# Performance work log

Measured on AMD Instinct MI355X. Metric: run time of the kernel, lower is better.

## Reference

```python
import jax, jax.numpy as jnp
import numpy as np

N = 131072          # total sampled proposals (flattened over batch)
D = 1024            # num_extractor_out
C = 21              # num_classes (VOC: 20 + background)


def setup_inputs() -> dict:
    key = jax.random.key(0)
    k1, k2, k3 = jax.random.split(key, 3)
    features = jax.random.normal(k1, (N, D), dtype=jnp.float32)
    # Linear weights stored as [in, out] so y = x @ W + b
    W_cls = jax.random.normal(k2, (D, C), dtype=jnp.float32) * (1.0 / np.sqrt(D))
    b_cls = jnp.zeros((C,), dtype=jnp.float32)
    W_tf = jax.random.normal(k3, (D, C * 4), dtype=jnp.float32) * (1.0 / np.sqrt(D))
    b_tf = jnp.zeros((C * 4,), dtype=jnp.float32)
    return {"features": features, "W_cls": W_cls, "b_cls": b_cls, "W_tf": W_tf, "b_tf": b_tf}


def reference(features, W_cls, b_cls, W_tf, b_tf):
    # ROI.forward with identity extractor / no pre/post transforms.
    proposal_classes = features @ W_cls + b_cls                    # [N, C]
    proposal_transformers = features @ W_tf + b_tf                 # [N, C*4]
    proposal_transformers = proposal_transformers.reshape(features.shape[0], C, 4)
    return proposal_classes, proposal_transformers
```

## Files before the change

### kernel.cpp

```cpp
#include <hip/hip_runtime.h>
#include <hip/hip_bf16.h>

#define NROWS 131072
#define DK    1024
#define CCLS  21
#define CTF   84
#define NCOL  105
#define NCT   7
#define BM    16
#define SLABF 256
#define NSLAB (DK / SLABF)

typedef __attribute__((ext_vector_type(4))) float f32x4;
typedef __attribute__((ext_vector_type(8))) short bf16x8;
typedef __attribute__((ext_vector_type(2))) unsigned int u32x2;

__device__ __forceinline__ unsigned short f2bf_rne(float x) {
    union { float f; unsigned u; } v; v.f = x;
    unsigned r = v.u + 0x7fffu + ((v.u >> 16) & 1u);
    return (unsigned short)(r >> 16);
}

__device__ __forceinline__ unsigned pack2(float lo, float hi) {
    union { float f; unsigned u; } a, b; a.f = lo; b.f = hi;
    return ((a.u + 0x8000u) >> 16) | ((b.u + 0x8000u) & 0xffff0000u);
}

__global__ void pack_B_kernel(const float* __restrict__ Wc,
                              const float* __restrict__ Wt,
                              unsigned short* __restrict__ Bp) {
    const int frag = blockIdx.x;
    const int kt = frag / NCT, ct = frag % NCT;
    const int lane = threadIdx.x;
    const int col = ct * 16 + (lane & 15);
    const int k0  = kt * 32 + ((lane >> 4) << 3);
    bf16x8 o;
#pragma unroll
    for (int j = 0; j < 8; ++j) {
        const int k = k0 + j;
        float v = 0.0f;
        if (col < CCLS)      v = Wc[k * CCLS + col];
        else if (col < NCOL) v = Wt[k * CTF + (col - CCLS)];
        o[j] = (short)f2bf_rne(v);
    }
    *reinterpret_cast<bf16x8*>(Bp + ((size_t)frag * 64 + lane) * 8) = o;
}

__global__ __launch_bounds__(256, 4)
void roi_gemm_kernel(const float* __restrict__ F,
                     const unsigned short* __restrict__ Bp,
                     const float* __restrict__ bcls,
                     const float* __restrict__ btf,
                     float* __restrict__ out) {
    __shared__ __align__(16) unsigned char smem[28672];

    const int t    = threadIdx.x;
    const int wave = t >> 6;
    const int lane = t & 63;
    const int fr   = lane & 15;
    const int fq   = lane >> 4;
    const long rw  = (long)blockIdx.x * BM;

    const unsigned short* bb = Bp + (size_t)lane * 8;
    const float* abase = F + (size_t)(rw + wave * 4) * DK + lane * 4;

    f32x4 acc[NCT];
#pragma unroll
    for (int ct = 0; ct < NCT; ++ct) acc[ct] = (f32x4){0.f, 0.f, 0.f, 0.f};

#define AWADDR(BUF, Q) (smem + (BUF) * 8192 + (wave * 4 + (Q)) * 512 +        \
    (((lane >> 1) ^ ((wave * 4 + (Q)) & 7)) << 4) + ((lane & 1) << 3))

    {
        f32x4 v0[4];
#pragma unroll
        for (int q = 0; q < 4; ++q)
            v0[q] = *reinterpret_cast<const f32x4*>(abase + (size_t)q * DK);
#pragma unroll
        for (int q = 0; q < 4; ++q) {
            u32x2 d;
            d[0] = pack2(v0[q][0], v0[q][1]);
            d[1] = pack2(v0[q][2], v0[q][3]);
            *reinterpret_cast<u32x2*>(AWADDR(0, q)) = d;
        }
    }
    __syncthreads();

#pragma unroll
    for (int s = 0; s < NSLAB; ++s) {
        const int buf = s & 1;

        bf16x8 bfr[2][NCT];
#pragma unroll
        for (int jj = 0; jj < 2; ++jj) {
            const int ktg = s * 8 + wave * 2 + jj;
#pragma unroll
            for (int ct = 0; ct < NCT; ++ct)
                bfr[jj][ct] = *reinterpret_cast<const bf16x8*>(
                    bb + ((size_t)(ktg * NCT + ct) * 512));
        }
        __builtin_amdgcn_sched_barrier(0);

        f32x4 v[4];
        if (s + 1 < NSLAB) {
#pragma unroll
            for (int q = 0; q < 4; ++q)
                v[q] = *reinterpret_cast<const f32x4*>(
                    abase + (size_t)q * DK + (s + 1) * SLABF);
        }
        __builtin_amdgcn_sched_barrier(0);

#pragma unroll
        for (int jj = 0; jj < 2; ++jj) {
            const int lt = wave * 2 + jj;
            const bf16x8 a = *reinterpret_cast<const bf16x8*>(
                smem + buf * 8192 + fr * 512 +
                ((((lt << 2) | fq) ^ (fr & 7)) << 4));
#pragma unroll
            for (int ct = 0; ct < NCT; ++ct)
                acc[ct] = __builtin_amdgcn_mfma_f32_16x16x32_bf16(
                    a, bfr[jj][ct], acc[ct], 0, 0, 0);
        }
        __builtin_amdgcn_sched_barrier(0);

        if (s + 1 < NSLAB) {
#pragma unroll
            for (int q = 0; q < 4; ++q) {
                u32x2 d;
                d[0] = pack2(v[q][0], v[q][1]);
                d[1] = pack2(v[q][2], v[q][3]);
                *reinterpret_cast<u32x2*>(AWADDR(buf ^ 1, q)) = d;
            }
        }
        __syncthreads();
    }
#undef AWADDR

    float* sf = reinterpret_cast<float*>(smem);
#pragma unroll
    for (int ct = 0; ct < NCT; ++ct)
        *reinterpret_cast<f32x4*>(sf + ((wave * NCT + ct) << 8) + (lane << 2)) =
            acc[ct];
    __syncthreads();

    const int rcol0 = (t >> 2) & 15;
    float* out_tf = out + (size_t)NROWS * CCLS;
    const long grow = rw + ((t >> 6) << 2) + (t & 3);
#pragma unroll
    for (int ct = 0; ct < NCT; ++ct) {
        const int col = ct * 16 + rcol0;
        if (col >= NCOL) continue;
        const float v = sf[(0 * NCT + ct) * 256 + t] +
                        sf[(1 * NCT + ct) * 256 + t] +
                        sf[(2 * NCT + ct) * 256 + t] +
                        sf[(3 * NCT + ct) * 256 + t] +
                        ((col < CCLS) ? bcls[col] : btf[col - CCLS]);
        if (col < CCLS) out[grow * CCLS + col] = v;
        else            out_tf[grow * CTF + (col - CCLS)] = v;
    }
}

extern "C" void kernel_launch(void* const* d_in, const int* in_sizes, int n_in,
                              void* d_out, int out_size, void* d_ws, size_t ws_size,
                              hipStream_t stream) {
    const float* F  = (const float*)d_in[0];
    const float* Wc = (const float*)d_in[1];
    const float* bc = (const float*)d_in[2];
    const float* Wt = (const float*)d_in[3];
    const float* bt = (const float*)d_in[4];
    unsigned short* Bp = (unsigned short*)d_ws;

    pack_B_kernel<<<NCT * (DK / 32), 64, 0, stream>>>(Wc, Wt, Bp);
    roi_gemm_kernel<<<NROWS / BM, 256, 0, stream>>>(F, Bp, bc, bt,
                                                    (float*)d_out);
}
```

Before: 145.1 us.

## Deepen software pipeline with smaller K slabs and prefetched B fragments

Halves the K slab to 128 so each wave handles one k-tile per slab, and restructures the main loop into an explicitly unrolled two-stage pipeline. A loads are issued two slabs ahead and B fragments one slab ahead in ping-pong registers, while the bf16 conversion writes to LDS happen after the MFMAs. The full __syncthreads is replaced by an lgkmcnt wait plus s_barrier. The goal is to hide global memory latency of this bandwidth-bound skinny GEMM behind the MFMAs, at the cost of more barriers per K and higher register pressure.

```diff
diff --git a/kernel.cpp b/kernel.cpp
--- a/kernel.cpp
+++ b/kernel.cpp
@@ -8,7 +8,7 @@
 #define NCOL  105
 #define NCT   7
 #define BM    16
-#define SLABF 256
+#define SLABF 128
 #define NSLAB (DK / SLABF)
 
 typedef __attribute__((ext_vector_type(4))) float f32x4;
@@ -62,80 +62,98 @@
     const long rw  = (long)blockIdx.x * BM;
 
     const unsigned short* bb = Bp + (size_t)lane * 8;
-    const float* abase = F + (size_t)(rw + wave * 4) * DK + lane * 4;
+    const float* asrc = F + (size_t)(rw + wave * 4 + (lane >> 5)) * DK
+                        + (lane & 31) * 4;
+
+    const int c   = (lane & 31) >> 1;
+    const int h8  = (lane & 1) << 3;
+    const int R0  = wave * 4 + (lane >> 5);
+    const int R1  = R0 + 2;
+    const int w0  = R0 * 256 + (((c) ^ (R0 & 7)) << 4) + h8;
+    const int w1  = R1 * 256 + (((c) ^ (R1 & 7)) << 4) + h8;
+    const int rdoff = fr * 256 + (((wave * 4 + fq) ^ (fr & 7)) << 4);
 
     f32x4 acc[NCT];
 #pragma unroll
     for (int ct = 0; ct < NCT; ++ct) acc[ct] = (f32x4){0.f, 0.f, 0.f, 0.f};
 
-#define AWADDR(BUF, Q) (smem + (BUF) * 8192 + (wave * 4 + (Q)) * 512 +        \
-    (((lane >> 1) ^ ((wave * 4 + (Q)) & 7)) << 4) + ((lane & 1) << 3))
+    f32x4 vP[2], vQ[2];
+    bf16x8 bfrP[NCT], bfrQ[NCT];
 
-    {
-        f32x4 v0[4];
-#pragma unroll
-        for (int q = 0; q < 4; ++q)
-            v0[q] = *reinterpret_cast<const f32x4*>(abase + (size_t)q * DK);
-#pragma unroll
-        for (int q = 0; q < 4; ++q) {
-            u32x2 d;
-            d[0] = pack2(v0[q][0], v0[q][1]);
-            d[1] = pack2(v0[q][2], v0[q][3]);
-            *reinterpret_cast<u32x2*>(AWADDR(0, q)) = d;
-        }
-    }
+#define LOADA(V, S) do {                                                      \
+    V[0] = *reinterpret_cast<const f32x4*>(asrc + (size_t)(S) * SLABF);       \
+    V[1] = *reinterpret_cast<const f32x4*>(asrc + (size_t)(S) * SLABF         \
+                                           + 2 * DK);                         \
+} while (0)
+
+#define LOADB(BF, S) do {                                                     \
+    const int ktg_ = (S) * 4 + wave;                                          \
+    _Pragma("unroll")                                                         \
+    for (int ct = 0; ct < NCT; ++ct)                                          \
+        BF[ct] = *reinterpret_cast<const bf16x8*>(                            \
+            bb + ((size_t)(ktg_ * NCT + ct) * 512));                          \
+} while (0)
+
+#define WRITEA(V, BUF) do {                                                   \
+    u32x2 d0_; d0_[0] = pack2(V[0][0], V[0][1]);                              \
+    d0_[1] = pack2(V[0][2], V[0][3]);                                         \
+    u32x2 d1_; d1_[0] = pack2(V[1][0], V[1][1]);                              \
+    d1_[1] = pack2(V[1][2], V[1][3]);                                         \
+    *reinterpret_cast<u32x2*>(smem + (BUF) * 4096 + w0) = d0_;                \
+    *reinterpret_cast<u32x2*>(smem + (BUF) * 4096 + w1) = d1_;                \
+} while (0)
+
+#define COMPUTE(BF, BUF) do {                                                 \
+    const bf16x8 a_ = *reinterpret_cast<const bf16x8*>(                       \
+        smem + (BUF) * 4096 + rdoff);                                         \
+    _Pragma("unroll")                                                         \
+    for (int ct = 0; ct < NCT; ++ct)                                          \
+        acc[ct] = __builtin_amdgcn_mfma_f32_16x16x32_bf16(                    \
+            a_, BF[ct], acc[ct], 0, 0, 0);                                    \
+} while (0)
+
+#define SLAB(S, BCUR, BNXT, VW, VL) do {                                      \
+    if ((S) + 1 < NSLAB) LOADB(BNXT, (S) + 1);                                \
+    __builtin_amdgcn_sched_barrier(0);                                        \
+    if ((S) + 2 < NSLAB) LOADA(VL, (S) + 2);                                  \
+    __builtin_amdgcn_sched_barrier(0);                                        \
+    COMPUTE(BCUR, (S) & 1);                                                   \
+    __builtin_amdgcn_sched_barrier(0);                                        \
+    if ((S) + 1 < NSLAB) {                                                    \
+        WRITEA(VW, ((S) + 1) & 1);                                            \
+        __builtin_amdgcn_sched_barrier(0);                                    \
+        asm volatile("s_waitcnt lgkmcnt(0)" ::: "memory");                    \
+        __builtin_amdgcn_s_barrier();                                         \
+        __builtin_amdgcn_sched_barrier(0);                                    \
+    }                                                                         \
+} while (0)
+
+    LOADA(vP, 0);
+    LOADA(vQ, 1);
+    LOADB(bfrP, 0);
+    __builtin_amdgcn_sched_barrier(0);
+    WRITEA(vP, 0);
+    __builtin_amdgcn_sched_barrier(0);
+    asm volatile("s_waitcnt lgkmcnt(0)" ::: "memory");
+    __builtin_amdgcn_s_barrier();
+    __builtin_amdgcn_sched_barrier(0);
+
+    SLAB(0, bfrP, bfrQ, vQ, vP);
+    SLAB(1, bfrQ, bfrP, vP, vQ);
+    SLAB(2, bfrP, bfrQ, vQ, vP);
+    SLAB(3, bfrQ, bfrP, vP, vQ);
+    SLAB(4, bfrP, bfrQ, vQ, vP);
+    SLAB(5, bfrQ, bfrP, vP, vQ);
+    SLAB(6, bfrP, bfrQ, vQ, vP);
+    SLAB(7, bfrQ, bfrP, vP, vQ);
+
+#undef SLAB
+#undef COMPUTE
+#undef WRITEA
+#undef LOADB
+#undef LOADA
+
     __syncthreads();
-
-#pragma unroll
-    for (int s = 0; s < NSLAB; ++s) {
-        const int buf = s & 1;
-
-        bf16x8 bfr[2][NCT];
-#pragma unroll
-        for (int jj = 0; jj < 2; ++jj) {
-            const int ktg = s * 8 + wave * 2 + jj;
-#pragma unroll
-            for (int ct = 0; ct < NCT; ++ct)
-                bfr[jj][ct] = *reinterpret_cast<const bf16x8*>(
-                    bb + ((size_t)(ktg * NCT + ct) * 512));
-        }
-        __builtin_amdgcn_sched_barrier(0);
-
-        f32x4 v[4];
-        if (s + 1 < NSLAB) {
-#pragma unroll
-            for (int q = 0; q < 4; ++q)
-                v[q] = *reinterpret_cast<const f32x4*>(
-                    abase + (size_t)q * DK + (s + 1) * SLABF);
-        }
-        __builtin_amdgcn_sched_barrier(0);
-
-#pragma unroll
-        for (int jj = 0; jj < 2; ++jj) {
-            const int lt = wave * 2 + jj;
-            const bf16x8 a = *reinterpret_cast<const bf16x8*>(
-                smem + buf * 8192 + fr * 512 +
-                ((((lt << 2) | fq) ^ (fr & 7)) << 4));
-#pragma unroll
-            for (int ct = 0; ct < NCT; ++ct)
-                acc[ct] = __builtin_amdgcn_mfma_f32_16x16x32_bf16(
-                    a, bfr[jj][ct], acc[ct], 0, 0, 0);
-        }
-        __builtin_amdgcn_sched_barrier(0);
-
-        if (s + 1 < NSLAB) {
-#pragma unroll
-            for (int q = 0; q < 4; ++q) {
-                u32x2 d;
-                d[0] = pack2(v[q][0], v[q][1]);
-                d[1] = pack2(v[q][2], v[q][3]);
-                *reinterpret_cast<u32x2*>(AWADDR(buf ^ 1, q)) = d;
-            }
-        }
-        __syncthreads();
-    }
-#undef AWADDR
-
     float* sf = reinterpret_cast<float*>(smem);
 #pragma unroll
     for (int ct = 0; ct < NCT; ++ct)
```

Result: slower. 162.1 us (+11.7%).

## Double rows per block so each B fragment feeds two MFMA row tiles

Applied to the files above, without the earlier changes.

Raises the block row tile from 16 to 32. Each wave now loads two A fragments per k-step and issues two MFMAs per B fragment, which halves B-fragment global/L2 traffic per output row and doubles the MFMA work per B load. LDS grows to 32 KB and the launch-bounds occupancy hint drops from 4 to 3 blocks per CU. The epilogue runs the cross-wave reduction twice, with extra barriers between the two passes.

```diff
diff --git a/kernel.cpp b/kernel.cpp
--- a/kernel.cpp
+++ b/kernel.cpp
@@ -7,7 +7,7 @@
 #define CTF   84
 #define NCOL  105
 #define NCT   7
-#define BM    16
+#define BM    32
 #define SLABF 256
 #define NSLAB (DK / SLABF)
 
@@ -46,13 +46,13 @@
     *reinterpret_cast<bf16x8*>(Bp + ((size_t)frag * 64 + lane) * 8) = o;
 }
 
-__global__ __launch_bounds__(256, 4)
+__global__ __launch_bounds__(256, 3)
 void roi_gemm_kernel(const float* __restrict__ F,
                      const unsigned short* __restrict__ Bp,
                      const float* __restrict__ bcls,
                      const float* __restrict__ btf,
                      float* __restrict__ out) {
-    __shared__ __align__(16) unsigned char smem[28672];
+    __shared__ __align__(16) unsigned char smem[32768];
 
     const int t    = threadIdx.x;
     const int wave = t >> 6;
@@ -62,22 +62,25 @@
     const long rw  = (long)blockIdx.x * BM;
 
     const unsigned short* bb = Bp + (size_t)lane * 8;
-    const float* abase = F + (size_t)(rw + wave * 4) * DK + lane * 4;
+    const float* abase = F + (size_t)(rw + wave * 8) * DK + lane * 4;
 
-    f32x4 acc[NCT];
+    f32x4 acc[2][NCT];
 #pragma unroll
-    for (int ct = 0; ct < NCT; ++ct) acc[ct] = (f32x4){0.f, 0.f, 0.f, 0.f};
+    for (int rt = 0; rt < 2; ++rt)
+#pragma unroll
+        for (int ct = 0; ct < NCT; ++ct)
+            acc[rt][ct] = (f32x4){0.f, 0.f, 0.f, 0.f};
 
-#define AWADDR(BUF, Q) (smem + (BUF) * 8192 + (wave * 4 + (Q)) * 512 +        \
-    (((lane >> 1) ^ ((wave * 4 + (Q)) & 7)) << 4) + ((lane & 1) << 3))
+#define AWADDR(BUF, Q) (smem + (BUF) * 16384 + (wave * 8 + (Q)) * 512 +       \
+    (((lane >> 1) ^ ((wave * 8 + (Q)) & 7)) << 4) + ((lane & 1) << 3))
 
     {
-        f32x4 v0[4];
+        f32x4 v0[8];
 #pragma unroll
-        for (int q = 0; q < 4; ++q)
+        for (int q = 0; q < 8; ++q)
             v0[q] = *reinterpret_cast<const f32x4*>(abase + (size_t)q * DK);
 #pragma unroll
-        for (int q = 0; q < 4; ++q) {
+        for (int q = 0; q < 8; ++q) {
             u32x2 d;
             d[0] = pack2(v0[q][0], v0[q][1]);
             d[1] = pack2(v0[q][2], v0[q][3]);
@@ -101,10 +104,10 @@
         }
         __builtin_amdgcn_sched_barrier(0);
 
-        f32x4 v[4];
+        f32x4 v[8];
         if (s + 1 < NSLAB) {
 #pragma unroll
-            for (int q = 0; q < 4; ++q)
+            for (int q = 0; q < 8; ++q)
                 v[q] = *reinterpret_cast<const f32x4*>(
                     abase + (size_t)q * DK + (s + 1) * SLABF);
         }
@@ -113,19 +116,25 @@
 #pragma unroll
         for (int jj = 0; jj < 2; ++jj) {
             const int lt = wave * 2 + jj;
-            const bf16x8 a = *reinterpret_cast<const bf16x8*>(
-                smem + buf * 8192 + fr * 512 +
-                ((((lt << 2) | fq) ^ (fr & 7)) << 4));
+            bf16x8 a[2];
 #pragma unroll
-            for (int ct = 0; ct < NCT; ++ct)
-                acc[ct] = __builtin_amdgcn_mfma_f32_16x16x32_bf16(
-                    a, bfr[jj][ct], acc[ct], 0, 0, 0);
+            for (int rt = 0; rt < 2; ++rt)
+                a[rt] = *reinterpret_cast<const bf16x8*>(
+                    smem + buf * 16384 + (rt * 16 + fr) * 512 +
+                    ((((lt << 2) | fq) ^ (fr & 7)) << 4));
+#pragma unroll
+            for (int ct = 0; ct < NCT; ++ct) {
+                acc[0][ct] = __builtin_amdgcn_mfma_f32_16x16x32_bf16(
+                    a[0], bfr[jj][ct], acc[0][ct], 0, 0, 0);
+                acc[1][ct] = __builtin_amdgcn_mfma_f32_16x16x32_bf16(
+                    a[1], bfr[jj][ct], acc[1][ct], 0, 0, 0);
+            }
         }
         __builtin_amdgcn_sched_barrier(0);
 
         if (s + 1 < NSLAB) {
 #pragma unroll
-            for (int q = 0; q < 4; ++q) {
+            for (int q = 0; q < 8; ++q) {
                 u32x2 d;
                 d[0] = pack2(v[q][0], v[q][1]);
                 d[1] = pack2(v[q][2], v[q][3]);
@@ -137,26 +146,31 @@
 #undef AWADDR
 
     float* sf = reinterpret_cast<float*>(smem);
-#pragma unroll
-    for (int ct = 0; ct < NCT; ++ct)
-        *reinterpret_cast<f32x4*>(sf + ((wave * NCT + ct) << 8) + (lane << 2)) =
-            acc[ct];
-    __syncthreads();
-
     const int rcol0 = (t >> 2) & 15;
     float* out_tf = out + (size_t)NROWS * CCLS;
-    const long grow = rw + ((t >> 6) << 2) + (t & 3);
+
 #pragma unroll
-    for (int ct = 0; ct < NCT; ++ct) {
-        const int col = ct * 16 + rcol0;
-        if (col >= NCOL) continue;
-        const float v = sf[(0 * NCT + ct) * 256 + t] +
-                        sf[(1 * NCT + ct) * 256 + t] +
-                        sf[(2 * NCT + ct) * 256 + t] +
-                        sf[(3 * NCT + ct) * 256 + t] +
-                        ((col < CCLS) ? bcls[col] : btf[col - CCLS]);
-        if (col < CCLS) out[grow * CCLS + col] = v;
-        else            out_tf[grow * CTF + (col - CCLS)] = v;
+    for (int rt = 0; rt < 2; ++rt) {
+#pragma unroll
+        for (int ct = 0; ct < NCT; ++ct)
+            *reinterpret_cast<f32x4*>(
+                sf + ((wave * NCT + ct) << 8) + (lane << 2)) = acc[rt][ct];
+        __syncthreads();
+
+        const long grow = rw + rt * 16 + ((t >> 6) << 2) + (t & 3);
+#pragma unroll
+        for (int ct = 0; ct < NCT; ++ct) {
+            const int col = ct * 16 + rcol0;
+            if (col >= NCOL) continue;
+            const float v = sf[(0 * NCT + ct) * 256 + t] +
+                            sf[(1 * NCT + ct) * 256 + t] +
+                            sf[(2 * NCT + ct) * 256 + t] +
+                            sf[(3 * NCT + ct) * 256 + t] +
+                            ((col < CCLS) ? bcls[col] : btf[col - CCLS]);
+            if (col < CCLS) out[grow * CCLS + col] = v;
+            else            out_tf[grow * CTF + (col - CCLS)] = v;
+        }
+        __syncthreads();
     }
 }
 
```

Result: slower. 172.1 us (+18.6%).
